# Kernel tuning notes

Hardware: AMD Instinct MI355X
Metric: run time of the kernel (lower is better)

## Reference

```python
import jax, jax.numpy as jnp
import numpy as np

N, B, H, C, NF = 200000, 100, 128, 3, 128


def setup_inputs() -> dict:
    key = jax.random.key(0)
    ks = jax.random.split(key, 12)
    def w(k, shape, s=0.05):
        return jax.random.normal(k, shape, jnp.float32) * s
    return dict(
        node_feat=w(ks[0], (N, NF), 1.0),
        coord=w(ks[1], (N, 3), 1.0),
        virtual_node_feat=w(ks[2], (B, NF, C), 1.0),
        virtual_coord=w(ks[3], (B, 3, C), 1.0),
        data_batch=jnp.sort(jax.random.randint(ks[4], (N,), 0, B)),
        We1=w(ks[5], (2 * NF + 1, H)), be1=jnp.zeros((H,), jnp.float32),
        We2=w(ks[6], (H, H)), be2=jnp.zeros((H,), jnp.float32),
        Wc1=w(ks[7], (H, H)), bc1=jnp.zeros((H,), jnp.float32),
        Wc2=w(ks[8], (H, 1), 0.001),  # xavier gain=0.001 layer, no bias
        Wn1=w(ks[9], (2 * H, H)), bn1=jnp.zeros((H,), jnp.float32),
        Wn2=w(ks[10], (H, H)), bn2=jnp.zeros((H,), jnp.float32),
    )


def _segment_mean(x, idx, num_segments):
    # x: [N, d1, d2] -> [num_segments, d1, d2]; mean over nodes of each graph
    sums = jax.ops.segment_sum(x, idx, num_segments=num_segments)
    counts = jax.ops.segment_sum(jnp.ones((x.shape[0],), x.dtype), idx,
                                 num_segments=num_segments)
    return sums / jnp.maximum(counts, 1.0)[:, None, None]


def reference(node_feat, coord, virtual_node_feat, virtual_coord, data_batch,
              We1, be1, We2, be2, Wc1, bc1, Wc2, Wn1, bn1, Wn2, bn2):
    silu = jax.nn.silu
    n, nf = node_feat.shape
    nb, _, c = virtual_coord.shape

    # gather: real node -> its graph's virtual nodes
    diff = virtual_coord[data_batch] - coord[:, :, None]            # [N,3,C]
    radial = jnp.linalg.norm(diff, axis=1)                          # [N,C]

    # edge model (work in [N,C,feat] layout to avoid permutes)
    feat_R = jnp.broadcast_to(node_feat[:, None, :], (n, c, nf))    # [N,C,NF]
    feat_V = virtual_node_feat[data_batch].transpose(0, 2, 1)       # [N,C,NF]
    e_in = jnp.concatenate([feat_R, feat_V, radial[:, :, None]], axis=-1)
    m = silu(e_in @ We1 + be1)
    m = silu(m @ We2 + be2)                                         # [N,C,H]

    # coord model: per (node, virtual-channel) scalar weight
    s = silu(m @ Wc1 + bc1) @ Wc2                                   # [N,C,1]
    trans = diff * s[:, :, 0][:, None, :]                           # [N,3,C]
    virtual_coord = virtual_coord + _segment_mean(trans, data_batch, nb)

    # node model on virtual nodes
    agg = _segment_mean(m, data_batch, nb)                          # [B,C,H]
    n_in = jnp.concatenate([virtual_node_feat.transpose(0, 2, 1), agg], axis=-1)
    h = silu(n_in @ Wn1 + bn1) @ Wn2 + bn2                          # [B,C,H]
    virtual_node_feat = virtual_node_feat + h.transpose(0, 2, 1)    # residual

    return virtual_node_feat, virtual_coord
```

## Files before the change

### kernel.cpp

```cpp
#include <hip/hip_runtime.h>
#include <hip/hip_bf16.h>
#include <math.h>

#define NNODES 200000
#define NGRAPH 100
#define HD     128
#define NCH    3
#define BN     64
#define EROWS  (BN*NCH)
#define ESTR   136


typedef short short8 __attribute__((ext_vector_type(8)));
typedef float f32x4  __attribute__((ext_vector_type(4)));

#define MFMA_16x16x32(a,b,c) __builtin_amdgcn_mfma_f32_16x16x32_bf16((a),(b),(c),0,0,0)

__device__ __forceinline__ float bf2f(unsigned short u) {
    return __uint_as_float(((unsigned int)u) << 16);
}
__device__ __forceinline__ unsigned short f2bf(float f) {
    return (unsigned short)((__float_as_uint(f) + 0x8000u) >> 16);
}
__device__ __forceinline__ float silu_f(float x) {
    return x * __builtin_amdgcn_rcpf(1.0f + __expf(-x));
}

__global__ void prep_kernel(const float* __restrict__ We1,
                            const float* __restrict__ We2,
                            const float* __restrict__ Wc1,
                            const float* __restrict__ be1,
                            const float* __restrict__ be2,
                            const float* __restrict__ bc1,
                            const float* __restrict__ Wc2,
                            const float* __restrict__ vnf,
                            unsigned short* __restrict__ w1r,
                            unsigned short* __restrict__ w2r,
                            unsigned short* __restrict__ wc1r,
                            float* __restrict__ Q,
                            float* __restrict__ wlast,
                            float* __restrict__ be1f,
                            float* __restrict__ be2f,
                            float* __restrict__ bc1f,
                            float* __restrict__ wc2f) {
    int bid = blockIdx.x;
    if (bid < 192) {
        int t = bid * 256 + threadIdx.x;
        int m  = t / 16384;
        int e  = t % 16384;
        int j  = e & 7;
        int l  = (e >> 3) & 63;
        int ks = (e >> 9) & 3;
        int ct = e >> 11;
        int row = ks * 32 + (l >> 4) * 8 + j;
        int col = ct * 16 + (l & 15);
        const float*    src = (m == 0) ? We1 : ((m == 1) ? We2 : Wc1);
        unsigned short* dst = (m == 0) ? w1r : ((m == 1) ? w2r : wc1r);
        dst[e] = f2bf(src[row * 128 + col]);
        if (t < 128) {
            wlast[t] = We1[256 * 128 + t];
            be1f[t]  = be1[t];
            be2f[t]  = be2[t];
            bc1f[t]  = bc1[t];
            wc2f[t]  = Wc2[t];
        }
    } else {
        int bc = bid - 192;
        int b = bc / NCH, c = bc % NCH;
        int t = threadIdx.x;
        __shared__ float v[128];
        if (t < 128) v[t] = vnf[(b * 128 + t) * 3 + c];
        __syncthreads();
        if (t < 128) {
            float s = 0.0f;
            for (int k = 0; k < 128; ++k)
                s += v[k] * We1[(128 + k) * 128 + t];
            Q[(b * 3 + c) * 128 + t] = s;
        }
    }
}

__global__ __launch_bounds__(256, 2) void egcl_main(
    const float* __restrict__ node_feat,
    const float* __restrict__ coord,
    const float* __restrict__ vcoord,
    const int*   __restrict__ batch,
    const unsigned short* __restrict__ w1r,
    const unsigned short* __restrict__ w2r,
    const unsigned short* __restrict__ wc1r,
    const float* __restrict__ Q,
    const float* __restrict__ wlast,
    const float* __restrict__ be1f,
    const float* __restrict__ be2f,
    const float* __restrict__ bc1f,
    const float* __restrict__ wc2f,
    float* __restrict__ aggsum,
    float* __restrict__ transsum,
    float* __restrict__ cnt)
{
    __shared__ __align__(16) unsigned short e_buf[EROWS * ESTR];
    __shared__ float sdiff[BN][3][3];
    __shared__ float sradial[BN][3];
    __shared__ float s_s[EROWS];
    __shared__ float sagg[NCH * HD];
    __shared__ unsigned short sbatch[BN];
    __shared__ unsigned short sseg_start[BN + 1];
    __shared__ unsigned short sseg_b[BN];
    __shared__ int snseg;

    const int tid   = threadIdx.x;
    const int wave  = tid >> 6;
    const int lane  = tid & 63;
    const int lrow  = lane & 15;
    const int lkb   = (lane >> 4) * 8;
    const int rq    = (lane >> 4) * 4;
    const int node0 = blockIdx.x * BN;

    for (int k = tid; k < NCH * HD; k += 256) sagg[k] = 0.0f;
    if (tid < BN) {
        int n = node0 + tid;
        int b = batch[n];
        sbatch[tid] = (unsigned short)b;
        int prev = (tid > 0) ? batch[n - 1] : -1;
        unsigned long long mask = __ballot(b != prev);
        int ns = __popcll(mask);
        if (b != prev) {
            int idx = __popcll(mask & ((1ull << tid) - 1ull));
            sseg_start[idx] = (unsigned short)tid;
            sseg_b[idx]     = (unsigned short)b;
        }
        if (tid == 0) { sseg_start[ns] = BN; snseg = ns; }
        float cx = coord[n * 3 + 0];
        float cy = coord[n * 3 + 1];
        float cz = coord[n * 3 + 2];
        for (int c = 0; c < 3; ++c) {
            float dx = vcoord[b * 9 + 0 * 3 + c] - cx;
            float dy = vcoord[b * 9 + 1 * 3 + c] - cy;
            float dz = vcoord[b * 9 + 2 * 3 + c] - cz;
            sdiff[tid][0][c] = dx;
            sdiff[tid][1][c] = dy;
            sdiff[tid][2][c] = dz;
            sradial[tid][c] = sqrtf(dx * dx + dy * dy + dz * dz);
        }
    }
    __syncthreads();
    const int nseg = snseg;

    f32x4 acc1[8] = {};
    {
        const float* arow = node_feat + (size_t)(node0 + wave * 16 + lrow) * 128;
        for (int ks = 0; ks < 4; ++ks) {
            f32x4 x0 = *(const f32x4*)(arow + ks * 32 + lkb);
            f32x4 x1 = *(const f32x4*)(arow + ks * 32 + lkb + 4);
            short8 af;
            af[0] = (short)f2bf(x0[0]); af[1] = (short)f2bf(x0[1]);
            af[2] = (short)f2bf(x0[2]); af[3] = (short)f2bf(x0[3]);
            af[4] = (short)f2bf(x1[0]); af[5] = (short)f2bf(x1[1]);
            af[6] = (short)f2bf(x1[2]); af[7] = (short)f2bf(x1[3]);
            for (int ct = 0; ct < 8; ++ct) {
                short8 bfg = *(const short8*)(w1r + ((ct * 4 + ks) * 64 + lane) * 8);
                acc1[ct] = MFMA_16x16x32(af, bfg, acc1[ct]);
            }
        }
    }
    for (int ct = 0; ct < 8; ++ct) {
        int h = ct * 16 + lrow;
        float wl = wlast[h];
        float bb = be1f[h];
        for (int r = 0; r < 4; ++r) {
            int nl = wave * 16 + rq + r;
            int b  = sbatch[nl];
            float p = acc1[ct][r] + bb;
            for (int c = 0; c < 3; ++c) {
                float x = p + Q[(b * 3 + c) * 128 + h] + sradial[nl][c] * wl;
                e_buf[(c * 64 + nl) * ESTR + h] = f2bf(silu_f(x));
            }
        }
    }

    f32x4 acc2[3][8] = {};
    for (int ks = 0; ks < 4; ++ks) {
        short8 af[3];
        for (int j = 0; j < 3; ++j)
            af[j] = *(const short8*)(&e_buf[(j * 64 + wave * 16 + lrow) * ESTR +
                                            ks * 32 + lkb]);
        for (int ct = 0; ct < 8; ++ct) {
            short8 bfg = *(const short8*)(w2r + ((ct * 4 + ks) * 64 + lane) * 8);
            for (int j = 0; j < 3; ++j)
                acc2[j][ct] = MFMA_16x16x32(af[j], bfg, acc2[j][ct]);
        }
    }
    for (int j = 0; j < 3; ++j) {
        for (int ct = 0; ct < 8; ++ct) {
            int h = ct * 16 + lrow;
            float bb = be2f[h];
            float psum = 0.0f;
            for (int r = 0; r < 4; ++r) {
                int row = j * 64 + wave * 16 + rq + r;
                unsigned short us = f2bf(silu_f(acc2[j][ct][r] + bb));
                e_buf[row * ESTR + h] = us;
                psum += bf2f(us);
            }
            if (nseg == 1) {
                psum += __shfl_xor(psum, 16, 64);
                psum += __shfl_xor(psum, 32, 64);
                if (lane < 16)
                    atomicAdd(&sagg[j * 128 + ct * 16 + lane], psum);
            }
        }
    }

    f32x4 acc3[3][8] = {};
    for (int ks = 0; ks < 4; ++ks) {
        short8 af[3];
        for (int j = 0; j < 3; ++j)
            af[j] = *(const short8*)(&e_buf[(j * 64 + wave * 16 + lrow) * ESTR +
                                            ks * 32 + lkb]);
        for (int ct = 0; ct < 8; ++ct) {
            short8 bfg = *(const short8*)(wc1r + ((ct * 4 + ks) * 64 + lane) * 8);
            for (int j = 0; j < 3; ++j)
                acc3[j][ct] = MFMA_16x16x32(af[j], bfg, acc3[j][ct]);
        }
    }
    for (int j = 0; j < 3; ++j) {
        float p0 = 0.f, p1 = 0.f, p2 = 0.f, p3 = 0.f;
        for (int ct = 0; ct < 8; ++ct) {
            int h = ct * 16 + lrow;
            float bb = bc1f[h];
            float w2 = wc2f[h];
            p0 += silu_f(acc3[j][ct][0] + bb) * w2;
            p1 += silu_f(acc3[j][ct][1] + bb) * w2;
            p2 += silu_f(acc3[j][ct][2] + bb) * w2;
            p3 += silu_f(acc3[j][ct][3] + bb) * w2;
        }
        for (int off = 1; off < 16; off <<= 1) {
            p0 += __shfl_xor(p0, off, 64);
            p1 += __shfl_xor(p1, off, 64);
            p2 += __shfl_xor(p2, off, 64);
            p3 += __shfl_xor(p3, off, 64);
        }
        if (lrow == 0) {
            int rbase = j * 64 + wave * 16 + rq;
            s_s[rbase + 0] = p0;
            s_s[rbase + 1] = p1;
            s_s[rbase + 2] = p2;
            s_s[rbase + 3] = p3;
        }
    }
    __syncthreads();

    if (nseg == 1) {
        int b = sseg_b[0];
        for (int idx = tid; idx < NCH * HD; idx += 256)
            atomicAdd(&aggsum[b * NCH * HD + idx], sagg[idx]);
    } else {
        for (int sg = 0; sg < nseg; ++sg) {
            int s0 = sseg_start[sg], s1 = sseg_start[sg + 1], b = sseg_b[sg];
            for (int idx = tid; idx < NCH * HD; idx += 256) {
                int c = idx >> 7, h = idx & 127;
                float sum = 0.f;
                for (int ii = s0; ii < s1; ++ii)
                    sum += bf2f(e_buf[(c * 64 + ii) * ESTR + h]);
                atomicAdd(&aggsum[(b * 3 + c) * 128 + h], sum);
            }
        }
    }
    for (int sg = 0; sg < nseg; ++sg) {
        int s0 = sseg_start[sg], s1 = sseg_start[sg + 1], b = sseg_b[sg];
        if (tid < 9) {
            int d = tid / 3, c = tid % 3;
            float sum = 0.f;
            for (int ii = s0; ii < s1; ++ii)
                sum += sdiff[ii][d][c] * s_s[c * 64 + ii];
            atomicAdd(&transsum[b * 9 + d * 3 + c], sum);
        }
        if (tid == 0) atomicAdd(&cnt[b], (float)(s1 - s0));
    }
}

__global__ void finalize_kernel(const float* __restrict__ vnf,
                                const float* __restrict__ vcoord,
                                const float* __restrict__ Wn1,
                                const float* __restrict__ bn1,
                                const float* __restrict__ Wn2,
                                const float* __restrict__ bn2,
                                const float* __restrict__ aggsum,
                                const float* __restrict__ transsum,
                                const float* __restrict__ cnt,
                                float* __restrict__ out) {
    int b = blockIdx.x / NCH;
    int c = blockIdx.x % NCH;
    int j = threadIdx.x;
    __shared__ float nin[256];
    __shared__ float h1[128];
    float count = fmaxf(cnt[b], 1.0f);
    nin[j]       = vnf[(b * 128 + j) * 3 + c];
    nin[128 + j] = aggsum[(b * 3 + c) * 128 + j] / count;
    __syncthreads();
    float x = bn1[j];
    for (int k = 0; k < 256; ++k)
        x += nin[k] * Wn1[k * 128 + j];
    h1[j] = silu_f(x);
    __syncthreads();
    float y = bn2[j];
    for (int k = 0; k < 128; ++k)
        y += h1[k] * Wn2[k * 128 + j];
    out[(b * 128 + j) * 3 + c] = vnf[(b * 128 + j) * 3 + c] + y;
    if (c == 0 && j < 9) {
        out[NGRAPH * 128 * 3 + b * 9 + j] =
            vcoord[b * 9 + j] + transsum[b * 9 + j] / count;
    }
}

extern "C" void kernel_launch(void* const* d_in, const int* in_sizes, int n_in,
                              void* d_out, int out_size, void* d_ws, size_t ws_size,
                              hipStream_t stream) {
    const float* node_feat = (const float*)d_in[0];
    const float* coord     = (const float*)d_in[1];
    const float* vnf       = (const float*)d_in[2];
    const float* vcoord    = (const float*)d_in[3];
    const int*   batch     = (const int*)d_in[4];
    const float* We1 = (const float*)d_in[5];
    const float* be1 = (const float*)d_in[6];
    const float* We2 = (const float*)d_in[7];
    const float* be2 = (const float*)d_in[8];
    const float* Wc1 = (const float*)d_in[9];
    const float* bc1 = (const float*)d_in[10];
    const float* Wc2 = (const float*)d_in[11];
    const float* Wn1 = (const float*)d_in[12];
    const float* bn1 = (const float*)d_in[13];
    const float* Wn2 = (const float*)d_in[14];
    const float* bn2 = (const float*)d_in[15];

    char* ws = (char*)d_ws;
    float*          aggsum   = (float*)(ws + 0);
    float*          transsum = (float*)(ws + 153600);
    float*          cntp     = (float*)(ws + 157200);
    float*          Q        = (float*)(ws + 157600);
    unsigned short* w1r      = (unsigned short*)(ws + 311200);
    unsigned short* w2r      = (unsigned short*)(ws + 343968);
    unsigned short* wc1r     = (unsigned short*)(ws + 376736);
    float*          wlast    = (float*)(ws + 409504);
    float*          be1f     = (float*)(ws + 410016);
    float*          be2f     = (float*)(ws + 410528);
    float*          bc1f     = (float*)(ws + 411040);
    float*          wc2f     = (float*)(ws + 411552);

    (void)hipMemsetAsync(d_ws, 0, 157600, stream);

    prep_kernel<<<192 + NGRAPH * NCH, 256, 0, stream>>>(
        We1, We2, Wc1, be1, be2, bc1, Wc2, vnf,
        w1r, w2r, wc1r, Q, wlast, be1f, be2f, bc1f, wc2f);

    egcl_main<<<NNODES / BN, 256, 0, stream>>>(
        node_feat, coord, vcoord, batch, w1r, w2r, wc1r, Q,
        wlast, be1f, be2f, bc1f, wc2f, aggsum, transsum, cntp);

    finalize_kernel<<<NGRAPH * NCH, 128, 0, stream>>>(
        vnf, vcoord, Wn1, bn1, Wn2, bn2, aggsum, transsum, cntp,
        (float*)d_out);
}
```

Measured before the change: 365.6 us.

## Stash diff/radial in e_buf padding, atomically accumulate aggregates directly to global

```diff
diff --git a/kernel.cpp b/kernel.cpp
--- a/kernel.cpp
+++ b/kernel.cpp
@@ -9,7 +9,6 @@
 #define BN     64
 #define EROWS  (BN*NCH)
 #define ESTR   136
-
 
 typedef short short8 __attribute__((ext_vector_type(8)));
 typedef float f32x4  __attribute__((ext_vector_type(4)));
@@ -99,10 +98,7 @@
     float* __restrict__ cnt)
 {
     __shared__ __align__(16) unsigned short e_buf[EROWS * ESTR];
-    __shared__ float sdiff[BN][3][3];
-    __shared__ float sradial[BN][3];
     __shared__ float s_s[EROWS];
-    __shared__ float sagg[NCH * HD];
     __shared__ unsigned short sbatch[BN];
     __shared__ unsigned short sseg_start[BN + 1];
     __shared__ unsigned short sseg_b[BN];
@@ -116,7 +112,6 @@
     const int rq    = (lane >> 4) * 4;
     const int node0 = blockIdx.x * BN;
 
-    for (int k = tid; k < NCH * HD; k += 256) sagg[k] = 0.0f;
     if (tid < BN) {
         int n = node0 + tid;
         int b = batch[n];
@@ -137,10 +132,10 @@
             float dx = vcoord[b * 9 + 0 * 3 + c] - cx;
             float dy = vcoord[b * 9 + 1 * 3 + c] - cy;
             float dz = vcoord[b * 9 + 2 * 3 + c] - cz;
-            sdiff[tid][0][c] = dx;
-            sdiff[tid][1][c] = dy;
-            sdiff[tid][2][c] = dz;
-            sradial[tid][c] = sqrtf(dx * dx + dy * dy + dz * dz);
+            f32x4 pad;
+            pad[0] = dx; pad[1] = dy; pad[2] = dz;
+            pad[3] = sqrtf(dx * dx + dy * dy + dz * dz);
+            *(f32x4*)&e_buf[(c * 64 + tid) * ESTR + 128] = pad;
         }
     }
     __syncthreads();
@@ -163,17 +158,51 @@
             }
         }
     }
-    for (int ct = 0; ct < 8; ++ct) {
-        int h = ct * 16 + lrow;
-        float wl = wlast[h];
-        float bb = be1f[h];
-        for (int r = 0; r < 4; ++r) {
-            int nl = wave * 16 + rq + r;
-            int b  = sbatch[nl];
-            float p = acc1[ct][r] + bb;
-            for (int c = 0; c < 3; ++c) {
-                float x = p + Q[(b * 3 + c) * 128 + h] + sradial[nl][c] * wl;
-                e_buf[(c * 64 + nl) * ESTR + h] = f2bf(silu_f(x));
+    {
+        float wl[8], bb[8];
+        #pragma unroll
+        for (int ct = 0; ct < 8; ++ct) {
+            wl[ct] = wlast[ct * 16 + lrow];
+            bb[ct] = be1f[ct * 16 + lrow];
+        }
+        if (nseg == 1) {
+            const float* qb = Q + (int)sseg_b[0] * (NCH * HD);
+            float qv[3][8];
+            #pragma unroll
+            for (int c = 0; c < 3; ++c)
+                #pragma unroll
+                for (int ct = 0; ct < 8; ++ct)
+                    qv[c][ct] = qb[c * 128 + ct * 16 + lrow];
+            #pragma unroll
+            for (int r = 0; r < 4; ++r) {
+                int nl = wave * 16 + rq + r;
+                #pragma unroll
+                for (int c = 0; c < 3; ++c) {
+                    int row = c * 64 + nl;
+                    float rad = *(const float*)&e_buf[row * ESTR + 134];
+                    #pragma unroll
+                    for (int ct = 0; ct < 8; ++ct) {
+                        float x = acc1[ct][r] + bb[ct] + qv[c][ct] + rad * wl[ct];
+                        e_buf[row * ESTR + ct * 16 + lrow] = f2bf(silu_f(x));
+                    }
+                }
+            }
+        } else {
+            #pragma unroll
+            for (int r = 0; r < 4; ++r) {
+                int nl = wave * 16 + rq + r;
+                int b  = sbatch[nl];
+                #pragma unroll
+                for (int c = 0; c < 3; ++c) {
+                    int row = c * 64 + nl;
+                    float rad = *(const float*)&e_buf[row * ESTR + 134];
+                    const float* qb = Q + (b * 3 + c) * 128;
+                    #pragma unroll
+                    for (int ct = 0; ct < 8; ++ct) {
+                        float x = acc1[ct][r] + bb[ct] + qb[ct * 16 + lrow] + rad * wl[ct];
+                        e_buf[row * ESTR + ct * 16 + lrow] = f2bf(silu_f(x));
+                    }
+                }
             }
         }
     }
@@ -190,22 +219,26 @@
                 acc2[j][ct] = MFMA_16x16x32(af[j], bfg, acc2[j][ct]);
         }
     }
-    for (int j = 0; j < 3; ++j) {
-        for (int ct = 0; ct < 8; ++ct) {
-            int h = ct * 16 + lrow;
-            float bb = be2f[h];
-            float psum = 0.0f;
-            for (int r = 0; r < 4; ++r) {
-                int row = j * 64 + wave * 16 + rq + r;
-                unsigned short us = f2bf(silu_f(acc2[j][ct][r] + bb));
-                e_buf[row * ESTR + h] = us;
-                psum += bf2f(us);
-            }
-            if (nseg == 1) {
-                psum += __shfl_xor(psum, 16, 64);
-                psum += __shfl_xor(psum, 32, 64);
-                if (lane < 16)
-                    atomicAdd(&sagg[j * 128 + ct * 16 + lane], psum);
+    {
+        const int bagg = (nseg == 1) ? (int)sseg_b[0] * (NCH * HD) : 0;
+        for (int j = 0; j < 3; ++j) {
+            for (int ct = 0; ct < 8; ++ct) {
+                int h = ct * 16 + lrow;
+                float bb = be2f[h];
+                float psum = 0.0f;
+                #pragma unroll
+                for (int r = 0; r < 4; ++r) {
+                    int row = j * 64 + wave * 16 + rq + r;
+                    float v = silu_f(acc2[j][ct][r] + bb);
+                    e_buf[row * ESTR + h] = f2bf(v);
+                    psum += v;
+                }
+                if (nseg == 1) {
+                    psum += __shfl_xor(psum, 16, 64);
+                    psum += __shfl_xor(psum, 32, 64);
+                    if (lane < 16)
+                        atomicAdd(&aggsum[bagg + j * 128 + ct * 16 + lane], psum);
+                }
             }
         }
     }
@@ -233,6 +266,7 @@
             p2 += silu_f(acc3[j][ct][2] + bb) * w2;
             p3 += silu_f(acc3[j][ct][3] + bb) * w2;
         }
+        #pragma unroll
         for (int off = 1; off < 16; off <<= 1) {
             p0 += __shfl_xor(p0, off, 64);
             p1 += __shfl_xor(p1, off, 64);
@@ -251,8 +285,29 @@
 
     if (nseg == 1) {
         int b = sseg_b[0];
-        for (int idx = tid; idx < NCH * HD; idx += 256)
-            atomicAdd(&aggsum[b * NCH * HD + idx], sagg[idx]);
+        if (wave == 0) {
+            float t[9];
+            #pragma unroll
+            for (int c = 0; c < 3; ++c) {
+                int row = c * 64 + lane;
+                float sv = s_s[row];
+                float dx = *(const float*)&e_buf[row * ESTR + 128];
+                float dy = *(const float*)&e_buf[row * ESTR + 130];
+                float dz = *(const float*)&e_buf[row * ESTR + 132];
+                t[0 * 3 + c] = dx * sv;
+                t[1 * 3 + c] = dy * sv;
+                t[2 * 3 + c] = dz * sv;
+            }
+            #pragma unroll
+            for (int off = 1; off < 64; off <<= 1)
+                #pragma unroll
+                for (int k = 0; k < 9; ++k)
+                    t[k] += __shfl_xor(t[k], off, 64);
+            if (lane < 9)
+                atomicAdd(&transsum[b * 9 + lane],
+                          __shfl(t[lane], 0, 64));
+            if (lane == 0) atomicAdd(&cnt[b], 64.0f);
+        }
     } else {
         for (int sg = 0; sg < nseg; ++sg) {
             int s0 = sseg_start[sg], s1 = sseg_start[sg + 1], b = sseg_b[sg];
@@ -263,18 +318,16 @@
                     sum += bf2f(e_buf[(c * 64 + ii) * ESTR + h]);
                 atomicAdd(&aggsum[(b * 3 + c) * 128 + h], sum);
             }
-        }
-    }
-    for (int sg = 0; sg < nseg; ++sg) {
-        int s0 = sseg_start[sg], s1 = sseg_start[sg + 1], b = sseg_b[sg];
-        if (tid < 9) {
-            int d = tid / 3, c = tid % 3;
-            float sum = 0.f;
-            for (int ii = s0; ii < s1; ++ii)
-                sum += sdiff[ii][d][c] * s_s[c * 64 + ii];
-            atomicAdd(&transsum[b * 9 + d * 3 + c], sum);
-        }
-        if (tid == 0) atomicAdd(&cnt[b], (float)(s1 - s0));
+            if (tid < 9) {
+                int d = tid / 3, c = tid % 3;
+                float sum = 0.f;
+                for (int ii = s0; ii < s1; ++ii)
+                    sum += (*(const float*)&e_buf[(c * 64 + ii) * ESTR + 128 + 2 * d])
+                           * s_s[c * 64 + ii];
+                atomicAdd(&transsum[b * 9 + d * 3 + c], sum);
+            }
+            if (tid == 0) atomicAdd(&cnt[b], (float)(s1 - s0));
+        }
     }
 }
 
```

After: 363.4 us. About the same (-0.6%).
